# Optimization experiments

Hardware: AMD Instinct MI355X
Metric: run time of the kernel (lower is better)

## Reference

```python
import jax, jax.numpy as jnp
import numpy as np

B, N, Q, D = 1, 6, 10000, 256
HEADS, LEVELS, NPTS, ZANCH = 8, 1, 8, 4  # NPTS = 2*n_points, ZANCH = num_points_in_pillar
HF, WF = 32, 88
HD = D // HEADS


def setup_inputs() -> dict:
    key = jax.random.key(0)
    ks = jax.random.split(key, 18)
    s = 1.0 / np.sqrt(D)
    inp = {
        'queries': jax.random.normal(ks[0], (B, N, Q, D), jnp.float32),
        'pos_emb': jax.random.normal(ks[1], (B, N, Q, D), jnp.float32),
        'lvl_emb': jax.random.normal(ks[2], (LEVELS, D), jnp.float32),
        'cam_emb': jax.random.normal(ks[3], (N, D), jnp.float32),
        'features0': jax.random.normal(ks[4], (B * N, D, HF, WF), jnp.float32),
        'reference_points_3D': jax.random.uniform(ks[5], (B, N, Q, ZANCH, 2), jnp.float32),
        'bev_mask': jax.random.randint(ks[6], (B, N, Q, ZANCH, 2), 0, 2).astype(bool),
        # MSDeformAttn3D params
        'W_value': jax.random.normal(ks[7], (D, D), jnp.float32) * s,
        'b_value': jnp.zeros((D,), jnp.float32),
        'W_off': jax.random.normal(ks[8], (HEADS * LEVELS * NPTS * 2, D), jnp.float32) * 0.01,
        'b_off': jax.random.uniform(ks[9], (HEADS * LEVELS * NPTS * 2,), jnp.float32, -2.0, 2.0),
        'W_attn': jax.random.normal(ks[10], (HEADS * LEVELS * NPTS, D), jnp.float32) * s,
        'b_attn': jnp.zeros((HEADS * LEVELS * NPTS,), jnp.float32),
        'W_inner': jax.random.normal(ks[11], (D, D), jnp.float32) * s,
        'b_inner': jnp.zeros((D,), jnp.float32),
        # SpatialCrossAttention.output_proj
        'W_out': jax.random.normal(ks[12], (D, D), jnp.float32) * s,
        'b_out': jnp.zeros((D,), jnp.float32),
    }
    return inp


def _bilinear(value_t, loc, H, W):
    # value_t: (bn, heads, H*W, hd); loc: (bn, q, heads, pts, 2) normalized to [0,1]
    bn, q, heads, pts, _ = loc.shape
    hd = value_t.shape[-1]
    # grid_sample(2*loc-1, align_corners=False) -> pixel coord = loc*size - 0.5
    x = loc[..., 0] * W - 0.5
    y = loc[..., 1] * H - 0.5
    x0 = jnp.floor(x); y0 = jnp.floor(y)
    dx = x - x0; dy = y - y0
    x0 = x0.astype(jnp.int32); y0 = y0.astype(jnp.int32)
    out = jnp.zeros((bn, heads, q * pts, hd), value_t.dtype)
    corners = ((0, 0, (1 - dx) * (1 - dy)), (1, 0, dx * (1 - dy)),
               (0, 1, (1 - dx) * dy), (1, 1, dx * dy))
    for ox, oy, w in corners:
        xi = x0 + ox; yi = y0 + oy
        valid = (xi >= 0) & (xi < W) & (yi >= 0) & (yi < H)  # zero padding
        wgt = jnp.where(valid, w, 0.0)
        idx = jnp.clip(yi, 0, H - 1) * W + jnp.clip(xi, 0, W - 1)  # (bn,q,heads,pts)
        idx_t = idx.transpose(0, 2, 1, 3).reshape(bn, heads, q * pts)
        g = jnp.take_along_axis(value_t, idx_t[..., None], axis=2)  # (bn,heads,q*pts,hd)
        wgt_t = wgt.transpose(0, 2, 1, 3).reshape(bn, heads, q * pts)
        out = out + g * wgt_t[..., None]
    return out.reshape(bn, heads, q, pts, hd)


def _forward(queries, pos_emb, lvl_emb, cam_emb, features0, reference_points_3D, bev_mask,
             W_value, b_value, W_off, b_off, W_attn, b_attn, W_inner, b_inner, W_out, b_out):
    b, n, q, d = queries.shape
    hf, wf = features0.shape[-2:]
    # flatten features + level/cam embeddings -> (b*n, hw, d)
    feat = features0.reshape(b, n, d, hf * wf)
    feat = feat + lvl_emb[0][None, None, :, None] + cam_emb[None, :, :, None]
    input_flatten = feat.transpose(0, 1, 3, 2).reshape(b * n, hf * wf, d)

    qp = (queries + pos_emb).reshape(b * n, q, d)
    ref = reference_points_3D.reshape(b * n, q, ZANCH, 2)

    # --- MSDeformAttn3D (single level) ---
    value = (input_flatten @ W_value.T + b_value).reshape(b * n, hf * wf, HEADS, HD)
    off = (qp @ W_off.T + b_off).reshape(b * n, q, HEADS, LEVELS, NPTS, 2)
    attw = jax.nn.softmax((qp @ W_attn.T + b_attn).reshape(b * n, q, HEADS, LEVELS * NPTS), axis=-1)
    attw = attw.reshape(b * n, q, HEADS, LEVELS, NPTS)
    normalizer = jnp.array([wf, hf], queries.dtype)  # (W, H)
    pts_per_z = NPTS // ZANCH
    off_z = off.reshape(b * n, q, HEADS, LEVELS, pts_per_z, ZANCH, 2)
    loc = ref[:, :, None, None, None, :, :] + off_z / normalizer
    loc = loc.reshape(b * n, q, HEADS, LEVELS, NPTS, 2)

    value_t = value.transpose(0, 2, 1, 3)  # (bn, heads, hw, hd)
    sampled = _bilinear(value_t, loc[:, :, :, 0], hf, wf)  # (bn,heads,q,pts,hd)
    attw_t = attw[:, :, :, 0].transpose(0, 2, 1, 3)  # (bn,heads,q,pts)
    out = jnp.einsum('bhqp,bhqpc->bqhc', attw_t, sampled).reshape(b * n, q, d)
    out = out @ W_inner.T + b_inner

    # --- scatter back per camera, normalize by hit count ---
    attn = out.reshape(b, n, q, d)
    # indexes come from batch 0's mask (as in the original code)
    hit = (bev_mask[0, :, :, :, 0].astype(jnp.int32).sum(-1) > 0).astype(queries.dtype)  # (n,q)
    slots = (attn * hit[None, :, :, None]).sum(1)  # (b,q,d)
    count = (bev_mask[..., 0].astype(jnp.int32).sum(-1) > 0).astype(queries.dtype).sum(1)
    count = jnp.clip(count, 1.0, None)  # (b,q)
    slots = slots / count[..., None]
    return slots @ W_out.T + b_out


def reference(queries, pos_emb, lvl_emb, cam_emb, features0, reference_points_3D, bev_mask,
              W_value, b_value, W_off, b_off, W_attn, b_attn, W_inner, b_inner, W_out, b_out):
    return _forward(queries, pos_emb, lvl_emb, cam_emb, features0, reference_points_3D, bev_mask,
                    W_value, b_value, W_off, b_off, W_attn, b_attn, W_inner, b_inner, W_out, b_out)
```

## Files before the change

### kernel.cpp

```cpp
#include <hip/hip_runtime.h>
#include <hip/hip_bf16.h>

#define BN     6
#define NQ     10000
#define DIM    256
#define HEADS  8
#define HDD    32
#define HF_    32
#define WF_    88
#define HW_    (HF_*WF_)
#define MTOT   (BN*NQ)

typedef __attribute__((ext_vector_type(8))) unsigned short ushort8_t;
typedef __attribute__((ext_vector_type(8))) short bf16x8;
typedef __attribute__((ext_vector_type(4))) float f32x4;

static __device__ inline unsigned short f2bf(float x) {
    __hip_bfloat16 b = __float2bfloat16(x);
    return *(unsigned short*)&b;
}

__global__ __launch_bounds__(256)
void k_wcvt(const float* __restrict__ Wv, const float* __restrict__ Wo,
            const float* __restrict__ Wa, const float* __restrict__ Wi,
            const float* __restrict__ Wz,
            unsigned short* __restrict__ Wv_bf, unsigned short* __restrict__ Woa_bf,
            unsigned short* __restrict__ Wi_bf, unsigned short* __restrict__ Wz_bf)
{
    const int i4 = (blockIdx.x*256 + threadIdx.x) * 4;
    if (i4 < 65536) {
        float4 v;
        ushort4 p;
        v = *(const float4*)(Wv+i4); p.x=f2bf(v.x);p.y=f2bf(v.y);p.z=f2bf(v.z);p.w=f2bf(v.w);
        *(ushort4*)(Wv_bf+i4) = p;
        v = *(const float4*)(Wi+i4); p.x=f2bf(v.x);p.y=f2bf(v.y);p.z=f2bf(v.z);p.w=f2bf(v.w);
        *(ushort4*)(Wi_bf+i4) = p;
        v = *(const float4*)(Wz+i4); p.x=f2bf(v.x);p.y=f2bf(v.y);p.z=f2bf(v.z);p.w=f2bf(v.w);
        *(ushort4*)(Wz_bf+i4) = p;
    }
    if (i4 < 32768) {
        float4 v = *(const float4*)(Wo+i4);
        ushort4 p; p.x=f2bf(v.x);p.y=f2bf(v.y);p.z=f2bf(v.z);p.w=f2bf(v.w);
        *(ushort4*)(Woa_bf+i4) = p;
    }
    if (i4 < 16384) {
        float4 v = *(const float4*)(Wa+i4);
        ushort4 p; p.x=f2bf(v.x);p.y=f2bf(v.y);p.z=f2bf(v.z);p.w=f2bf(v.w);
        *(ushort4*)(Woa_bf+32768+i4) = p;
    }
}

__global__ __launch_bounds__(256)
void k_ebias(const float* __restrict__ lvl, const float* __restrict__ cam,
             const float* __restrict__ Wv, const float* __restrict__ bv,
             float* __restrict__ ebias)
{
    const int n = blockIdx.x;
    const int j = threadIdx.x;
    __shared__ float e[DIM];
    e[j] = lvl[j] + cam[n*DIM + j];
    __syncthreads();
    const float* w = Wv + (size_t)j*DIM;
    float s = bv[j];
    for (int d = 0; d < DIM; ++d) s += e[d]*w[d];
    ebias[n*DIM + j] = s;
}

__global__ __launch_bounds__(256)
void k_mask(const int* __restrict__ bev, float* __restrict__ hitf,
            float* __restrict__ scale, float* __restrict__ biasf)
{
    const int q = blockIdx.x*256 + threadIdx.x;
    if (q >= NQ) return;
    float cnt = 0.f;
    #pragma unroll
    for (int n = 0; n < BN; ++n) {
        int hit = 0;
        #pragma unroll
        for (int z = 0; z < 4; ++z)
            hit |= (bev[(((size_t)n*NQ + q)*4 + z)*2] != 0);
        hitf[(size_t)n*NQ + q] = (float)hit;
        cnt += (float)hit;
    }
    biasf[q] = (cnt > 0.f) ? 1.f : 0.f;
    scale[q] = 1.f / fmaxf(cnt, 1.f);
}

__global__ __launch_bounds__(256)
void k_feat(const float* __restrict__ feat, unsigned short* __restrict__ featT)
{
    __shared__ float Tf[64][68];
    const int cam = blockIdx.z;
    const int d0 = blockIdx.y * 64;
    const int p0 = blockIdx.x * 64;
    const int tid = threadIdx.x;
    #pragma unroll
    for (int i = 0; i < 4; ++i) {
        const int d = (tid>>4) + i*16;
        const int p4 = (tid&15)*4;
        *(float4*)&Tf[d][p4] = *(const float4*)(feat + ((size_t)cam*DIM + d0 + d)*HW_ + p0 + p4);
    }
    __syncthreads();
    const int p = tid>>2, dq = tid&3;
    unsigned short* ob = featT + ((size_t)cam*HW_ + p0 + p)*DIM + d0;
    #pragma unroll
    for (int i = 0; i < 4; ++i) {
        const int d4 = dq*4 + i*16;
        ushort4 pk;
        pk.x = f2bf(Tf[d4+0][p]); pk.y = f2bf(Tf[d4+1][p]);
        pk.z = f2bf(Tf[d4+2][p]); pk.w = f2bf(Tf[d4+3][p]);
        *(ushort4*)(ob + d4) = pk;
    }
}

__global__ __launch_bounds__(256)
void k_value_mfma(const unsigned short* __restrict__ featT,
                  const unsigned short* __restrict__ Wv_bf,
                  const float* __restrict__ ebias,
                  unsigned short* __restrict__ value_bf)
{
    __shared__ unsigned short Ap[128][72];
    __shared__ unsigned short Bc[64][72];
    const int cam = blockIdx.z;
    const int p0 = blockIdx.x * 128;
    const int c0 = blockIdx.y * 64;
    const int tid = threadIdx.x;
    const int lane = tid & 63, wave = tid >> 6;
    const int quad = lane >> 4, l15 = lane & 15;
    f32x4 acc[2][4] = {};
    const unsigned short* fbase = featT + ((size_t)cam*HW_ + p0)*DIM;

    for (int k0 = 0; k0 < DIM; k0 += 64) {
        #pragma unroll
        for (int i = 0; i < 4; ++i) {
            const int row = (tid>>3) + i*32;
            const int k8 = (tid&7)*8;
            *(ushort8_t*)&Ap[row][k8] = *(const ushort8_t*)(fbase + (size_t)row*DIM + k0 + k8);
        }
        #pragma unroll
        for (int i = 0; i < 2; ++i) {
            const int row = (tid>>3) + i*32;
            const int k8 = (tid&7)*8;
            *(ushort8_t*)&Bc[row][k8] = *(const ushort8_t*)(Wv_bf + (size_t)(c0+row)*DIM + k0 + k8);
        }
        __syncthreads();
        #pragma unroll
        for (int s = 0; s < 2; ++s) {
            const int kf = s*32 + quad*8;
            bf16x8 a[2], b[4];
            #pragma unroll
            for (int mt = 0; mt < 2; ++mt)
                a[mt] = *(const bf16x8*)&Ap[(wave*2+mt)*16 + l15][kf];
            #pragma unroll
            for (int nt = 0; nt < 4; ++nt)
                b[nt] = *(const bf16x8*)&Bc[nt*16 + l15][kf];
            #pragma unroll
            for (int mt = 0; mt < 2; ++mt)
                #pragma unroll
                for (int nt = 0; nt < 4; ++nt)
                    acc[mt][nt] = __builtin_amdgcn_mfma_f32_16x16x32_bf16(a[mt], b[nt], acc[mt][nt], 0,0,0);
        }
        __syncthreads();
    }
    #pragma unroll
    for (int nt = 0; nt < 4; ++nt) {
        const int c = c0 + nt*16 + l15;
        const float eb = ebias[cam*DIM + c];
        const int h = c >> 5, cc = c & 31;
        unsigned short* vb = value_bf + (size_t)(cam*HEADS + h)*HW_*HDD + cc;
        #pragma unroll
        for (int mt = 0; mt < 2; ++mt)
            #pragma unroll
            for (int r = 0; r < 4; ++r) {
                const int p = p0 + (wave*2+mt)*16 + quad*4 + r;
                vb[(size_t)p*HDD] = f2bf(acc[mt][nt][r] + eb);
            }
    }
}

__global__ __launch_bounds__(256)
void k_offattn(const float* __restrict__ Qr, const float* __restrict__ Pe,
               const unsigned short* __restrict__ Woa_bf,
               const float* __restrict__ boff, const float* __restrict__ battn,
               float* __restrict__ off_ws, float* __restrict__ attw_ws)
{
    __shared__ unsigned short Aq[64][72];
    __shared__ unsigned short Bw[192][72];
    const int m0 = blockIdx.x * 64;
    const int tid = threadIdx.x;
    const int lane = tid & 63, wave = tid >> 6;
    const int quad = lane >> 4, l15 = lane & 15;
    f32x4 acc[4][3] = {};
    const int n0 = wave * 48;
    const int srow = tid >> 2;
    const int sk4  = (tid & 3) * 4;

    for (int k0 = 0; k0 < DIM; k0 += 64) {
        const int m = m0 + srow;
        #pragma unroll
        for (int i = 0; i < 4; ++i) {
            const int kk = sk4 + i*16;
            float4 x = make_float4(0.f,0.f,0.f,0.f), y = x;
            if (m < MTOT) {
                x = *(const float4*)(Qr + (size_t)m*DIM + k0 + kk);
                y = *(const float4*)(Pe + (size_t)m*DIM + k0 + kk);
            }
            ushort4 pk;
            pk.x = f2bf(x.x+y.x); pk.y = f2bf(x.y+y.y);
            pk.z = f2bf(x.z+y.z); pk.w = f2bf(x.w+y.w);
            *(ushort4*)&Aq[srow][kk] = pk;
        }
        #pragma unroll
        for (int s = 0; s < 6; ++s) {
            const int row = (tid>>3) + s*32;
            const int k8 = (tid&7)*8;
            *(ushort8_t*)&Bw[row][k8] =
                *(const ushort8_t*)(Woa_bf + (size_t)row*DIM + k0 + k8);
        }
        __syncthreads();
        #pragma unroll
        for (int s = 0; s < 2; ++s) {
            const int kf = s*32 + quad*8;
            bf16x8 a[4], b[3];
            #pragma unroll
            for (int mt = 0; mt < 4; ++mt)
                a[mt] = *(const bf16x8*)&Aq[mt*16 + l15][kf];
            #pragma unroll
            for (int nt = 0; nt < 3; ++nt)
                b[nt] = *(const bf16x8*)&Bw[n0 + nt*16 + l15][kf];
            #pragma unroll
            for (int mt = 0; mt < 4; ++mt)
                #pragma unroll
                for (int nt = 0; nt < 3; ++nt)
                    acc[mt][nt] = __builtin_amdgcn_mfma_f32_16x16x32_bf16(a[mt], b[nt], acc[mt][nt], 0,0,0);
        }
        __syncthreads();
    }
    #pragma unroll
    for (int nt = 0; nt < 3; ++nt) {
        const int col = n0 + nt*16 + l15;
        const float bias = (col < 128) ? boff[col] : battn[col-128];
        #pragma unroll
        for (int mt = 0; mt < 4; ++mt) {
            #pragma unroll
            for (int r = 0; r < 4; ++r) {
                const int m = m0 + mt*16 + quad*4 + r;
                if (m >= MTOT) continue;
                const float v = acc[mt][nt][r] + bias;
                if (col < 128) off_ws [(size_t)m*128 + col]       = v;
                else           attw_ws[(size_t)m*64 + (col-128)]  = v;
            }
        }
    }
}

__global__ __launch_bounds__(256)
void k_sample(const unsigned short* __restrict__ value_bf,
              const float* __restrict__ off_ws, const float* __restrict__ attw_ws,
              const float* __restrict__ ref3d, const float* __restrict__ hitf,
              const float* __restrict__ scale, unsigned short* __restrict__ asum_bf)
{
    const int q0 = blockIdx.x * 8;
    const int tid = threadIdx.x;

    __shared__ float s_off[8][128];
    __shared__ float s_att[8][64];
    __shared__ float s_ref[8][8];
    __shared__ float s_hit[BN][8];
    __shared__ float s_scl[8];

    if (tid < 48) s_hit[tid>>3][tid&7] = hitf[(size_t)(tid>>3)*NQ + q0 + (tid&7)];
    if (tid < 8)  s_scl[tid] = scale[q0 + tid];

    const int quarter = tid & 3;
    const int h  = (tid >> 2) & 7;
    const int ql = tid >> 5;

    float acc[8];
    #pragma unroll
    for (int c = 0; c < 8; ++c) acc[c] = 0.f;

    for (int n = 0; n < BN; ++n) {
        __syncthreads();
        {
            const float4* so = (const float4*)(off_ws + ((size_t)n*NQ + q0)*128);
            ((float4*)&s_off[0][0])[tid] = so[tid];
            const float2* sa = (const float2*)(attw_ws + ((size_t)n*NQ + q0)*64);
            ((float2*)&s_att[0][0])[tid] = sa[tid];
            if (tid < 64)
                (&s_ref[0][0])[tid] = (ref3d + ((size_t)n*NQ + q0)*8)[tid];
        }
        __syncthreads();

        if (s_hit[n][ql] != 0.f) {
            float lg[8];
            float mx = -1e30f;
            #pragma unroll
            for (int p = 0; p < 8; ++p) { lg[p] = s_att[ql][h*8+p]; mx = fmaxf(mx, lg[p]); }
            float ssum = 0.f;
            #pragma unroll
            for (int p = 0; p < 8; ++p) { lg[p] = __expf(lg[p]-mx); ssum += lg[p]; }
            const float inv = 1.f/ssum;

            const unsigned short* vbase =
                value_bf + (size_t)(n*HEADS + h)*HW_*HDD + quarter*8;

            #pragma unroll
            for (int p = 0; p < 8; ++p) {
                const int z = p & 3;
                const float ax = s_ref[ql][z*2+0]*WF_ + s_off[ql][h*16+p*2+0] - 0.5f;
                const float ay = s_ref[ql][z*2+1]*HF_ + s_off[ql][h*16+p*2+1] - 0.5f;
                const float fx = floorf(ax), fy = floorf(ay);
                const float dx = ax-fx, dy = ay-fy;
                const int x0 = (int)fx, y0 = (int)fy;
                const float wp = lg[p]*inv;
                #pragma unroll
                for (int oy = 0; oy < 2; ++oy) {
                    const int yi = y0 + oy;
                    const float wy = oy ? dy : 1.f-dy;
                    #pragma unroll
                    for (int ox = 0; ox < 2; ++ox) {
                        const int xi = x0 + ox;
                        const float wx = ox ? dx : 1.f-dx;
                        const bool valid = ((unsigned)xi < WF_) & ((unsigned)yi < HF_);
                        const float cw = valid ? wp*wy*wx : 0.f;
                        const int xc = min(max(xi, 0), WF_-1);
                        const int yc = min(max(yi, 0), HF_-1);
                        const ushort8_t v = *(const ushort8_t*)(vbase + (size_t)(yc*WF_ + xc)*HDD);
                        #pragma unroll
                        for (int c = 0; c < 8; ++c)
                            acc[c] += cw * __uint_as_float(((unsigned)v[c]) << 16);
                    }
                }
            }
        }
    }

    const float sc = s_scl[ql];
    ushort8_t o;
    #pragma unroll
    for (int c = 0; c < 8; ++c) o[c] = f2bf(acc[c]*sc);
    *(ushort8_t*)(asum_bf + ((size_t)(q0+ql))*DIM + h*HDD + quarter*8) = o;
}

__global__ __launch_bounds__(256)
void k_gemm_mfma(const unsigned short* __restrict__ A_bf,
                 const unsigned short* __restrict__ W_bf,
                 const float* __restrict__ bias, const float* __restrict__ rowscale,
                 float* __restrict__ out_f, unsigned short* __restrict__ out_b, int M)
{
    __shared__ unsigned short As[128][72];
    __shared__ unsigned short Bs[64][72];
    const int m0 = blockIdx.x * 128;
    const int j0 = blockIdx.y * 64;
    const int tid = threadIdx.x;
    const int lane = tid & 63, wave = tid >> 6;
    const int quad = lane >> 4, l15 = lane & 15;
    f32x4 acc[2][4] = {};

    for (int k0 = 0; k0 < DIM; k0 += 64) {
        #pragma unroll
        for (int i = 0; i < 4; ++i) {
            const int row = (tid>>3) + i*32;
            const int k8 = (tid&7)*8;
            ushort8_t v = {0,0,0,0,0,0,0,0};
            if (m0 + row < M)
                v = *(const ushort8_t*)(A_bf + (size_t)(m0+row)*DIM + k0 + k8);
            *(ushort8_t*)&As[row][k8] = v;
        }
        #pragma unroll
        for (int i = 0; i < 2; ++i) {
            const int row = (tid>>3) + i*32;
            const int k8 = (tid&7)*8;
            *(ushort8_t*)&Bs[row][k8] = *(const ushort8_t*)(W_bf + (size_t)(j0+row)*DIM + k0 + k8);
        }
        __syncthreads();
        #pragma unroll
        for (int s = 0; s < 2; ++s) {
            const int kf = s*32 + quad*8;
            bf16x8 a[2], b[4];
            #pragma unroll
            for (int mt = 0; mt < 2; ++mt)
                a[mt] = *(const bf16x8*)&As[(wave*2+mt)*16 + l15][kf];
            #pragma unroll
            for (int nt = 0; nt < 4; ++nt)
                b[nt] = *(const bf16x8*)&Bs[nt*16 + l15][kf];
            #pragma unroll
            for (int mt = 0; mt < 2; ++mt)
                #pragma unroll
                for (int nt = 0; nt < 4; ++nt)
                    acc[mt][nt] = __builtin_amdgcn_mfma_f32_16x16x32_bf16(a[mt], b[nt], acc[mt][nt], 0,0,0);
        }
        __syncthreads();
    }
    #pragma unroll
    for (int nt = 0; nt < 4; ++nt) {
        const int j = j0 + nt*16 + l15;
        const float bj = bias[j];
        #pragma unroll
        for (int mt = 0; mt < 2; ++mt) {
            #pragma unroll
            for (int r = 0; r < 4; ++r) {
                const int m = m0 + (wave*2+mt)*16 + quad*4 + r;
                if (m >= M) continue;
                const float f = rowscale ? rowscale[m] : 1.f;
                const float v = acc[mt][nt][r] + f*bj;
                if (out_f) out_f[(size_t)m*DIM + j] = v;
                if (out_b) out_b[(size_t)m*DIM + j] = f2bf(v);
            }
        }
    }
}

extern "C" void kernel_launch(void* const* d_in, const int* in_sizes, int n_in,
                              void* d_out, int out_size, void* d_ws, size_t ws_size,
                              hipStream_t stream)
{
    const float* queries = (const float*)d_in[0];
    const float* pos_emb = (const float*)d_in[1];
    const float* lvl_emb = (const float*)d_in[2];
    const float* cam_emb = (const float*)d_in[3];
    const float* features= (const float*)d_in[4];
    const float* ref3d   = (const float*)d_in[5];
    const int*   bev     = (const int*)d_in[6];
    const float* Wv = (const float*)d_in[7];
    const float* bv = (const float*)d_in[8];
    const float* Wo = (const float*)d_in[9];
    const float* bo = (const float*)d_in[10];
    const float* Wa = (const float*)d_in[11];
    const float* ba = (const float*)d_in[12];
    const float* Wi = (const float*)d_in[13];
    const float* bi = (const float*)d_in[14];
    const float* Wz = (const float*)d_in[15];
    const float* bz = (const float*)d_in[16];
    float* out = (float*)d_out;

    char* ws = (char*)d_ws;
    size_t o = 0;
    auto alloc = [&](size_t bytes) { char* p = ws + o; o += (bytes + 255) & ~size_t(255); return p; };
    unsigned short* value_bf = (unsigned short*)alloc((size_t)BN*HEADS*HW_*HDD*2);
    unsigned short* featT    = (unsigned short*)alloc((size_t)BN*HW_*DIM*2);
    float* off_ws   = (float*)alloc((size_t)MTOT*128*4);
    float* attw_ws  = (float*)alloc((size_t)MTOT*64*4);
    unsigned short* asum_bf  = (unsigned short*)alloc((size_t)NQ*DIM*2);
    unsigned short* slots_bf = (unsigned short*)alloc((size_t)NQ*DIM*2);
    unsigned short* Wv_bf  = (unsigned short*)alloc(65536*2);
    unsigned short* Woa_bf = (unsigned short*)alloc(49152*2);
    unsigned short* Wi_bf  = (unsigned short*)alloc(65536*2);
    unsigned short* Wz_bf  = (unsigned short*)alloc(65536*2);
    float* hitf   = (float*)alloc((size_t)BN*NQ*4);
    float* scalev = (float*)alloc(NQ*4);
    float* biasf  = (float*)alloc(NQ*4);
    float* ebias  = (float*)alloc(BN*DIM*4);

    k_wcvt  <<<64, 256, 0, stream>>>(Wv, Wo, Wa, Wi, Wz, Wv_bf, Woa_bf, Wi_bf, Wz_bf);
    k_ebias <<<BN, 256, 0, stream>>>(lvl_emb, cam_emb, Wv, bv, ebias);
    k_mask  <<<(NQ+255)/256, 256, 0, stream>>>(bev, hitf, scalev, biasf);
    k_feat  <<<dim3(HW_/64, DIM/64, BN), 256, 0, stream>>>(features, featT);
    k_value_mfma<<<dim3(HW_/128, DIM/64, BN), 256, 0, stream>>>(featT, Wv_bf, ebias, value_bf);
    k_offattn<<<(MTOT+63)/64, 256, 0, stream>>>(queries, pos_emb, Woa_bf, bo, ba, off_ws, attw_ws);
    k_sample <<<NQ/8, 256, 0, stream>>>(value_bf, off_ws, attw_ws, ref3d, hitf, scalev, asum_bf);
    k_gemm_mfma<<<dim3((NQ+127)/128, DIM/64), 256, 0, stream>>>(asum_bf, Wi_bf, bi, biasf, nullptr, slots_bf, NQ);
    k_gemm_mfma<<<dim3((NQ+127)/128, DIM/64), 256, 0, stream>>>(slots_bf, Wz_bf, bz, nullptr, out, nullptr, NQ);
}
```

Measured before the change: 342.8 us.

## Drop shared memory staging in offset/attn GEMM and sampling kernels

The offset/attention projection kernel now assigns one 16-row strip per wave, holds the full A fragment (query+pos summed into bf16) in registers, and reads weight fragments straight from global/L2 with no LDS tiles or barriers. The sampling kernel drops its shared staging and per-camera __syncthreads, so each thread loads its own offsets, attention logits and reference points directly with vector loads and skips cameras that miss. The aim is to remove barrier stalls and LDS traffic. In exchange, global and L2 reads grow because weights and per-query data are no longer shared across threads in a block, and register pressure goes up.

Result: slower. 366.3 us (+6.9%).

```diff
diff --git a/kernel.cpp b/kernel.cpp
--- a/kernel.cpp
+++ b/kernel.cpp
@@ -184,72 +184,53 @@
                const float* __restrict__ boff, const float* __restrict__ battn,
                float* __restrict__ off_ws, float* __restrict__ attw_ws)
 {
-    __shared__ unsigned short Aq[64][72];
-    __shared__ unsigned short Bw[192][72];
-    const int m0 = blockIdx.x * 64;
     const int tid = threadIdx.x;
-    const int lane = tid & 63, wave = tid >> 6;
+    const int wave = tid >> 6, lane = tid & 63;
     const int quad = lane >> 4, l15 = lane & 15;
-    f32x4 acc[4][3] = {};
-    const int n0 = wave * 48;
-    const int srow = tid >> 2;
-    const int sk4  = (tid & 3) * 4;
-
-    for (int k0 = 0; k0 < DIM; k0 += 64) {
-        const int m = m0 + srow;
-        #pragma unroll
-        for (int i = 0; i < 4; ++i) {
-            const int kk = sk4 + i*16;
-            float4 x = make_float4(0.f,0.f,0.f,0.f), y = x;
-            if (m < MTOT) {
-                x = *(const float4*)(Qr + (size_t)m*DIM + k0 + kk);
-                y = *(const float4*)(Pe + (size_t)m*DIM + k0 + kk);
-            }
-            ushort4 pk;
-            pk.x = f2bf(x.x+y.x); pk.y = f2bf(x.y+y.y);
-            pk.z = f2bf(x.z+y.z); pk.w = f2bf(x.w+y.w);
-            *(ushort4*)&Aq[srow][kk] = pk;
-        }
-        #pragma unroll
-        for (int s = 0; s < 6; ++s) {
-            const int row = (tid>>3) + s*32;
-            const int k8 = (tid&7)*8;
-            *(ushort8_t*)&Bw[row][k8] =
-                *(const ushort8_t*)(Woa_bf + (size_t)row*DIM + k0 + k8);
-        }
-        __syncthreads();
-        #pragma unroll
-        for (int s = 0; s < 2; ++s) {
-            const int kf = s*32 + quad*8;
-            bf16x8 a[4], b[3];
-            #pragma unroll
-            for (int mt = 0; mt < 4; ++mt)
-                a[mt] = *(const bf16x8*)&Aq[mt*16 + l15][kf];
-            #pragma unroll
-            for (int nt = 0; nt < 3; ++nt)
-                b[nt] = *(const bf16x8*)&Bw[n0 + nt*16 + l15][kf];
-            #pragma unroll
-            for (int mt = 0; mt < 4; ++mt)
-                #pragma unroll
-                for (int nt = 0; nt < 3; ++nt)
-                    acc[mt][nt] = __builtin_amdgcn_mfma_f32_16x16x32_bf16(a[mt], b[nt], acc[mt][nt], 0,0,0);
-        }
-        __syncthreads();
-    }
-    #pragma unroll
-    for (int nt = 0; nt < 3; ++nt) {
-        const int col = n0 + nt*16 + l15;
+    const int m0 = (blockIdx.x*4 + wave) * 16;
+    if (m0 >= MTOT) return;
+
+    bf16x8 afr[8];
+    {
+        const float* qrow = Qr + (size_t)(m0 + l15)*DIM;
+        const float* prow = Pe + (size_t)(m0 + l15)*DIM;
+        #pragma unroll
+        for (int kc = 0; kc < 8; ++kc) {
+            const int k = kc*32 + quad*8;
+            const float4 x0 = *(const float4*)(qrow + k);
+            const float4 x1 = *(const float4*)(qrow + k + 4);
+            const float4 y0 = *(const float4*)(prow + k);
+            const float4 y1 = *(const float4*)(prow + k + 4);
+            ushort8_t u;
+            u[0]=f2bf(x0.x+y0.x); u[1]=f2bf(x0.y+y0.y); u[2]=f2bf(x0.z+y0.z); u[3]=f2bf(x0.w+y0.w);
+            u[4]=f2bf(x1.x+y1.x); u[5]=f2bf(x1.y+y1.y); u[6]=f2bf(x1.z+y1.z); u[7]=f2bf(x1.w+y1.w);
+            afr[kc] = *(bf16x8*)&u;
+        }
+    }
+
+    f32x4 acc[12] = {};
+    const unsigned short* bbase = Woa_bf + (size_t)l15*DIM + quad*8;
+    #pragma unroll
+    for (int kc = 0; kc < 8; ++kc) {
+        bf16x8 b[12];
+        #pragma unroll
+        for (int nt = 0; nt < 12; ++nt)
+            b[nt] = *(const bf16x8*)(bbase + (size_t)nt*16*DIM + kc*32);
+        #pragma unroll
+        for (int nt = 0; nt < 12; ++nt)
+            acc[nt] = __builtin_amdgcn_mfma_f32_16x16x32_bf16(afr[kc], b[nt], acc[nt], 0,0,0);
+    }
+
+    #pragma unroll
+    for (int nt = 0; nt < 12; ++nt) {
+        const int col = nt*16 + l15;
         const float bias = (col < 128) ? boff[col] : battn[col-128];
         #pragma unroll
-        for (int mt = 0; mt < 4; ++mt) {
-            #pragma unroll
-            for (int r = 0; r < 4; ++r) {
-                const int m = m0 + mt*16 + quad*4 + r;
-                if (m >= MTOT) continue;
-                const float v = acc[mt][nt][r] + bias;
-                if (col < 128) off_ws [(size_t)m*128 + col]       = v;
-                else           attw_ws[(size_t)m*64 + (col-128)]  = v;
-            }
+        for (int r = 0; r < 4; ++r) {
+            const int m = m0 + quad*4 + r;
+            const float v = acc[nt][r] + bias;
+            if (col < 128) off_ws [(size_t)m*128 + col]      = v;
+            else           attw_ws[(size_t)m*64 + (col-128)] = v;
         }
     }
 }
@@ -260,87 +241,77 @@
               const float* __restrict__ ref3d, const float* __restrict__ hitf,
               const float* __restrict__ scale, unsigned short* __restrict__ asum_bf)
 {
-    const int q0 = blockIdx.x * 8;
-    const int tid = threadIdx.x;
-
-    __shared__ float s_off[8][128];
-    __shared__ float s_att[8][64];
-    __shared__ float s_ref[8][8];
-    __shared__ float s_hit[BN][8];
-    __shared__ float s_scl[8];
-
-    if (tid < 48) s_hit[tid>>3][tid&7] = hitf[(size_t)(tid>>3)*NQ + q0 + (tid&7)];
-    if (tid < 8)  s_scl[tid] = scale[q0 + tid];
-
-    const int quarter = tid & 3;
-    const int h  = (tid >> 2) & 7;
-    const int ql = tid >> 5;
+    const int gtid = blockIdx.x*256 + threadIdx.x;
+    const int quarter = gtid & 3;
+    const int h  = (gtid >> 2) & 7;
+    const int q  = gtid >> 5;
 
     float acc[8];
     #pragma unroll
     for (int c = 0; c < 8; ++c) acc[c] = 0.f;
 
+    #pragma unroll 1
     for (int n = 0; n < BN; ++n) {
-        __syncthreads();
-        {
-            const float4* so = (const float4*)(off_ws + ((size_t)n*NQ + q0)*128);
-            ((float4*)&s_off[0][0])[tid] = so[tid];
-            const float2* sa = (const float2*)(attw_ws + ((size_t)n*NQ + q0)*64);
-            ((float2*)&s_att[0][0])[tid] = sa[tid];
-            if (tid < 64)
-                (&s_ref[0][0])[tid] = (ref3d + ((size_t)n*NQ + q0)*8)[tid];
-        }
-        __syncthreads();
-
-        if (s_hit[n][ql] != 0.f) {
-            float lg[8];
-            float mx = -1e30f;
-            #pragma unroll
-            for (int p = 0; p < 8; ++p) { lg[p] = s_att[ql][h*8+p]; mx = fmaxf(mx, lg[p]); }
-            float ssum = 0.f;
-            #pragma unroll
-            for (int p = 0; p < 8; ++p) { lg[p] = __expf(lg[p]-mx); ssum += lg[p]; }
-            const float inv = 1.f/ssum;
-
-            const unsigned short* vbase =
-                value_bf + (size_t)(n*HEADS + h)*HW_*HDD + quarter*8;
-
-            #pragma unroll
-            for (int p = 0; p < 8; ++p) {
-                const int z = p & 3;
-                const float ax = s_ref[ql][z*2+0]*WF_ + s_off[ql][h*16+p*2+0] - 0.5f;
-                const float ay = s_ref[ql][z*2+1]*HF_ + s_off[ql][h*16+p*2+1] - 0.5f;
-                const float fx = floorf(ax), fy = floorf(ay);
-                const float dx = ax-fx, dy = ay-fy;
-                const int x0 = (int)fx, y0 = (int)fy;
-                const float wp = lg[p]*inv;
+        if (hitf[(size_t)n*NQ + q] == 0.f) continue;
+        const size_t base = (size_t)n*NQ + q;
+
+        const float4 a0 = *(const float4*)(attw_ws + base*64 + h*8);
+        const float4 a1 = *(const float4*)(attw_ws + base*64 + h*8 + 4);
+        float lg[8] = {a0.x,a0.y,a0.z,a0.w, a1.x,a1.y,a1.z,a1.w};
+        float mx = -1e30f;
+        #pragma unroll
+        for (int p = 0; p < 8; ++p) mx = fmaxf(mx, lg[p]);
+        float ssum = 0.f;
+        #pragma unroll
+        for (int p = 0; p < 8; ++p) { lg[p] = __expf(lg[p]-mx); ssum += lg[p]; }
+        const float inv = 1.f/ssum;
+
+        float off[16];
+        #pragma unroll
+        for (int i = 0; i < 4; ++i)
+            *(float4*)&off[i*4] = *(const float4*)(off_ws + base*128 + h*16 + i*4);
+        float ref[8];
+        *(float4*)&ref[0] = *(const float4*)(ref3d + base*8);
+        *(float4*)&ref[4] = *(const float4*)(ref3d + base*8 + 4);
+
+        const unsigned short* vbase =
+            value_bf + (size_t)(n*HEADS + h)*HW_*HDD + quarter*8;
+
+        #pragma unroll
+        for (int p = 0; p < 8; ++p) {
+            const int z = p & 3;
+            const float ax = ref[z*2+0]*WF_ + off[p*2+0] - 0.5f;
+            const float ay = ref[z*2+1]*HF_ + off[p*2+1] - 0.5f;
+            const float fx = floorf(ax), fy = floorf(ay);
+            const float dx = ax-fx, dy = ay-fy;
+            const int x0 = (int)fx, y0 = (int)fy;
+            const float wp = lg[p]*inv;
+            #pragma unroll
+            for (int oy = 0; oy < 2; ++oy) {
+                const int yi = y0 + oy;
+                const float wy = oy ? dy : 1.f-dy;
                 #pragma unroll
-                for (int oy = 0; oy < 2; ++oy) {
-                    const int yi = y0 + oy;
-                    const float wy = oy ? dy : 1.f-dy;
+                for (int ox = 0; ox < 2; ++ox) {
+                    const int xi = x0 + ox;
+                    const float wx = ox ? dx : 1.f-dx;
+                    const bool valid = ((unsigned)xi < WF_) & ((unsigned)yi < HF_);
+                    const float cw = valid ? wp*wy*wx : 0.f;
+                    const int xc = min(max(xi, 0), WF_-1);
+                    const int yc = min(max(yi, 0), HF_-1);
+                    const ushort8_t v = *(const ushort8_t*)(vbase + (size_t)(yc*WF_ + xc)*HDD);
                     #pragma unroll
-                    for (int ox = 0; ox < 2; ++ox) {
-                        const int xi = x0 + ox;
-                        const float wx = ox ? dx : 1.f-dx;
-                        const bool valid = ((unsigned)xi < WF_) & ((unsigned)yi < HF_);
-                        const float cw = valid ? wp*wy*wx : 0.f;
-                        const int xc = min(max(xi, 0), WF_-1);
-                        const int yc = min(max(yi, 0), HF_-1);
-                        const ushort8_t v = *(const ushort8_t*)(vbase + (size_t)(yc*WF_ + xc)*HDD);
-                        #pragma unroll
-                        for (int c = 0; c < 8; ++c)
-                            acc[c] += cw * __uint_as_float(((unsigned)v[c]) << 16);
-                    }
+                    for (int c = 0; c < 8; ++c)
+                        acc[c] += cw * __uint_as_float(((unsigned)v[c]) << 16);
                 }
             }
         }
     }
 
-    const float sc = s_scl[ql];
+    const float sc = scale[q];
     ushort8_t o;
     #pragma unroll
     for (int c = 0; c < 8; ++c) o[c] = f2bf(acc[c]*sc);
-    *(ushort8_t*)(asum_bf + ((size_t)(q0+ql))*DIM + h*HDD + quarter*8) = o;
+    *(ushort8_t*)(asum_bf + (size_t)q*DIM + h*HDD + quarter*8) = o;
 }
 
 __global__ __launch_bounds__(256)
@@ -458,8 +429,8 @@
     k_mask  <<<(NQ+255)/256, 256, 0, stream>>>(bev, hitf, scalev, biasf);
     k_feat  <<<dim3(HW_/64, DIM/64, BN), 256, 0, stream>>>(features, featT);
     k_value_mfma<<<dim3(HW_/128, DIM/64, BN), 256, 0, stream>>>(featT, Wv_bf, ebias, value_bf);
-    k_offattn<<<(MTOT+63)/64, 256, 0, stream>>>(queries, pos_emb, Woa_bf, bo, ba, off_ws, attw_ws);
-    k_sample <<<NQ/8, 256, 0, stream>>>(value_bf, off_ws, attw_ws, ref3d, hitf, scalev, asum_bf);
+    k_offattn<<<(MTOT/16 + 3)/4, 256, 0, stream>>>(queries, pos_emb, Woa_bf, bo, ba, off_ws, attw_ws);
+    k_sample <<<NQ*32/256, 256, 0, stream>>>(value_bf, off_ws, attw_ws, ref3d, hitf, scalev, asum_bf);
     k_gemm_mfma<<<dim3((NQ+127)/128, DIM/64), 256, 0, stream>>>(asum_bf, Wi_bf, bi, biasf, nullptr, slots_bf, NQ);
     k_gemm_mfma<<<dim3((NQ+127)/128, DIM/64), 256, 0, stream>>>(slots_bf, Wz_bf, bz, nullptr, out, nullptr, NQ);
 }
```
